# Performance work log

Hardware: AMD Instinct MI355X
Metric: run time of the kernel (lower is better)

The kernel has to match this reference:

```python
import jax, jax.numpy as jnp
import numpy as np
import math

B, S, H, DK = 16, 4096, 16, 64
DM = H * DK          # 1024, d_model
QD = 1024            # q_d_model
KVD = 1024           # kv_d_model
MASK_P = 0.85        # randbool probability


def setup_inputs() -> dict:
    key = jax.random.key(0)
    ks = jax.random.split(key, 12)
    s = 0.02
    return {
        "q": jax.random.normal(ks[0], (B, 1, QD), jnp.float32),
        "k": jax.random.normal(ks[1], (B, S, KVD), jnp.float32),
        "v": jax.random.normal(ks[2], (B, S, KVD), jnp.float32),
        "Wq": jax.random.normal(ks[3], (QD, DM), jnp.float32) * s,
        "bq": jnp.zeros((DM,), jnp.float32),
        "Wk": jax.random.normal(ks[4], (KVD, DM), jnp.float32) * s,
        "bk": jnp.zeros((DM,), jnp.float32),
        "Wv": jax.random.normal(ks[5], (KVD, DM), jnp.float32) * s,
        "bv": jnp.zeros((DM,), jnp.float32),
        "Wo": jax.random.normal(ks[6], (DM, QD), jnp.float32) * s,
        "bo": jnp.zeros((QD,), jnp.float32),
        # randbool(shape, p=0.85): True where rand < p -> score zeroed
        "maskfill": jax.random.uniform(ks[7], (B, H, 1, S)) < MASK_P,
    }


def reference(q, k, v, Wq, bq, Wk, bk, Wv, bv, Wo, bo, maskfill):
    bs = q.shape[0]
    # projections -> [B, L, H, DK] -> [B, H, L, DK]
    qh = (q @ Wq + bq).reshape(bs, -1, H, DK).transpose(0, 2, 1, 3)  # [B,H,1,DK]
    kh = (k @ Wk + bk).reshape(bs, -1, H, DK).transpose(0, 2, 1, 3)  # [B,H,S,DK]
    vh = (v @ Wv + bv).reshape(bs, -1, H, DK).transpose(0, 2, 1, 3)  # [B,H,S,DK]

    scores1 = jnp.einsum("bhqd,bhkd->bhqk", qh, kh) / math.sqrt(DK)  # [B,H,1,S]

    # plain path (dropout = identity in eval)
    attn = jax.nn.softmax(scores1, axis=-1)
    out_h = jnp.einsum("bhqk,bhkd->bhqd", attn, vh)                  # [B,H,1,DK]

    # masked path: zero-fill (not -inf) masked raw scores, then softmax
    masked_scores = jnp.where(maskfill, 0.0, scores1)
    mattn = jax.nn.softmax(masked_scores, axis=-1)
    mout_h = jnp.einsum("bhqk,bhkd->bhqd", mattn, vh)

    concat = out_h.transpose(0, 2, 1, 3).reshape(bs, DM)
    mconcat = mout_h.transpose(0, 2, 1, 3).reshape(bs, DM)
    output = concat @ Wo + bo
    masked_output = mconcat @ Wo + bo
    return (output, masked_output)
```

## Files before the change

kernel.cpp:

```cpp
#include <hip/hip_runtime.h>
#include <stdint.h>

#define NB 16
#define NS 4096
#define NH 16
#define NC 1024

#define OFF_QHP   0u
#define OFF_QK    262144u
#define OFF_QB    524288u
#define OFF_SP    524608u
#define OFF_CTXP  532800u
#define OFF_CON   8921408u

__global__ __launch_bounds__(128) void k_qh(
    const float* __restrict__ q, const float* __restrict__ Wq, float* __restrict__ qhp)
{
    __shared__ float qs[64*16];
    int dz = blockIdx.x, cs = blockIdx.y;
    int tid = threadIdx.x;
    int d = dz*128 + tid;
#pragma unroll
    for (int j = 0; j < 2; ++j) {
        int idx = j*128 + tid;
        int b = idx >> 4, c4 = (idx & 15) << 2;
        float4 t = *(const float4*)(q + (size_t)b*NC + cs*64 + c4);
        qs[(c4+0)*16 + b] = t.x; qs[(c4+1)*16 + b] = t.y;
        qs[(c4+2)*16 + b] = t.z; qs[(c4+3)*16 + b] = t.w;
    }
    __syncthreads();
    float acc[16];
#pragma unroll
    for (int b = 0; b < 16; ++b) acc[b] = 0.f;
#pragma unroll 4
    for (int c = 0; c < 64; ++c) {
        float w = Wq[(size_t)(cs*64 + c)*NC + d];
        const float4* qr = (const float4*)(qs + c*16);
        float4 q0 = qr[0], q1 = qr[1], q2 = qr[2], q3 = qr[3];
        acc[0]  = fmaf(w, q0.x, acc[0]);  acc[1]  = fmaf(w, q0.y, acc[1]);
        acc[2]  = fmaf(w, q0.z, acc[2]);  acc[3]  = fmaf(w, q0.w, acc[3]);
        acc[4]  = fmaf(w, q1.x, acc[4]);  acc[5]  = fmaf(w, q1.y, acc[5]);
        acc[6]  = fmaf(w, q1.z, acc[6]);  acc[7]  = fmaf(w, q1.w, acc[7]);
        acc[8]  = fmaf(w, q2.x, acc[8]);  acc[9]  = fmaf(w, q2.y, acc[9]);
        acc[10] = fmaf(w, q2.z, acc[10]); acc[11] = fmaf(w, q2.w, acc[11]);
        acc[12] = fmaf(w, q3.x, acc[12]); acc[13] = fmaf(w, q3.y, acc[13]);
        acc[14] = fmaf(w, q3.z, acc[14]); acc[15] = fmaf(w, q3.w, acc[15]);
    }
#pragma unroll
    for (int b = 0; b < 16; ++b) qhp[((size_t)cs*16 + b)*NC + d] = acc[b];
}

__global__ __launch_bounds__(128) void k_qk(
    const float* __restrict__ qhp, const float* __restrict__ bq,
    const float* __restrict__ Wk, const float* __restrict__ bk,
    float* __restrict__ qko, float* __restrict__ qbv)
{
    int h = blockIdx.x;
    int c = blockIdx.y*128 + threadIdx.x;
    __shared__ float qs[16*64];
    for (int j = 0; j < 8; ++j) {
        int idx = j*128 + threadIdx.x;
        int b = idx >> 6, dd = idx & 63;
        float a = bq[h*64 + dd];
#pragma unroll
        for (int cs = 0; cs < 16; ++cs) a += qhp[((size_t)cs*16 + b)*NC + h*64 + dd];
        qs[idx] = a;
    }
    __syncthreads();
    const float* wr = Wk + (size_t)c*NC + h*64;
    float acc[16];
#pragma unroll
    for (int b = 0; b < 16; ++b) acc[b] = 0.f;
#pragma unroll 4
    for (int d = 0; d < 64; ++d) {
        float w = wr[d];
#pragma unroll
        for (int b = 0; b < 16; ++b) acc[b] = fmaf(qs[b*64 + d], w, acc[b]);
    }
#pragma unroll
    for (int b = 0; b < 16; ++b) qko[((size_t)b*NH + h)*NC + c] = acc[b];
    if (blockIdx.y == 0 && threadIdx.x < 16) {
        int b = threadIdx.x; float a = 0.f;
        for (int d = 0; d < 64; ++d) a = fmaf(qs[b*64 + d], bk[h*64 + d], a);
        qbv[b*NH + h] = a;
    }
}

#define QTS 20
#define SCOMP(BUF, W)                                                          \
    _Pragma("unroll")                                                          \
    for (int j = 0; j < 4; ++j) {                                              \
        const float* qp = qt + ((W)*16 + ph*4 + j)*QTS + hg*4;                 \
        float4 qv = *(const float4*)qp;                                        \
        _Pragma("unroll")                                                      \
        for (int i = 0; i < 8; ++i) {                                          \
            float kc = (j == 0) ? BUF[i].x : (j == 1) ? BUF[i].y               \
                     : (j == 2) ? BUF[i].z : BUF[i].w;                         \
            acc[i][0] = fmaf(kc, qv.x, acc[i][0]);                             \
            acc[i][1] = fmaf(kc, qv.y, acc[i][1]);                             \
            acc[i][2] = fmaf(kc, qv.z, acc[i][2]);                             \
            acc[i][3] = fmaf(kc, qv.w, acc[i][3]);                             \
        }                                                                      \
    }
__global__ __launch_bounds__(512, 2) void k_att(
    const float* __restrict__ kk, const float* __restrict__ vv,
    const float* __restrict__ qkm, const float* __restrict__ qbv,
    const void* __restrict__ mask, float* __restrict__ ctxp, float* __restrict__ Sp)
{
    __shared__ float qt[512*QTS];
    __shared__ float attl[256*32];
    __shared__ float red[8][2][16];
    int sb = blockIdx.x, b = blockIdx.y;
    int tid = threadIdx.x;
    int ph = tid & 3, hg = (tid >> 2) & 3, rg = tid >> 4;
    int srow = sb*256 + rg*8;

    int fl;
    {
        const uint4* mw = (const uint4*)mask;
        unsigned f = 0u, g = 0u;
#pragma unroll
        for (int j = 0; j < 8; ++j) {
            uint4 m4 = mw[j];
            f |= (m4.x == 0x3F800000u) | (m4.y == 0x3F800000u)
               | (m4.z == 0x3F800000u) | (m4.w == 0x3F800000u);
            g |= ((m4.x > 1u) & (m4.x != 0x3F800000u))
               | ((m4.y > 1u) & (m4.y != 0x3F800000u))
               | ((m4.z > 1u) & (m4.z != 0x3F800000u))
               | ((m4.w > 1u) & (m4.w != 0x3F800000u));
        }
        fl = f ? 2 : (g ? 1 : 0);
    }

    const float* kr = kk + ((size_t)b*NS + srow)*NC + ph*4;
    float acc[8][4];
#pragma unroll
    for (int i = 0; i < 8; ++i)
#pragma unroll
        for (int j = 0; j < 4; ++j) acc[i][j] = 0.f;

    for (int cz = 0; cz < 2; ++cz) {
        __syncthreads();
#pragma unroll
        for (int j = 0; j < 16; ++j) {
            int idx = j*512 + tid;
            int h = idx >> 9, c = idx & 511;
            qt[c*QTS + h] = qkm[((size_t)b*NH + h)*NC + cz*512 + c];
        }
        __syncthreads();
        const float* kc0 = kr + cz*512;
        float4 kv[8], kn[8];
#pragma unroll
        for (int i = 0; i < 8; ++i) kv[i] = *(const float4*)(kc0 + i*NC);
        for (int w = 0; w < 32; ++w) {
            if (w < 31) {
#pragma unroll
                for (int i = 0; i < 8; ++i)
                    kn[i] = *(const float4*)(kc0 + i*NC + (w+1)*16);
            }
            SCOMP(kv, w);
#pragma unroll
            for (int i = 0; i < 8; ++i) kv[i] = kn[i];
        }
    }
#pragma unroll
    for (int i = 0; i < 8; ++i)
#pragma unroll
        for (int j = 0; j < 4; ++j) {
            acc[i][j] += __shfl_xor(acc[i][j], 1, 64);
            acc[i][j] += __shfl_xor(acc[i][j], 2, 64);
        }
    float d0[4], d1[4];
    if (ph == 0) {
#pragma unroll
        for (int j = 0; j < 4; ++j) { d0[j] = acc[0][j]; d1[j] = acc[1][j]; }
    } else if (ph == 1) {
#pragma unroll
        for (int j = 0; j < 4; ++j) { d0[j] = acc[2][j]; d1[j] = acc[3][j]; }
    } else if (ph == 2) {
#pragma unroll
        for (int j = 0; j < 4; ++j) { d0[j] = acc[4][j]; d1[j] = acc[5][j]; }
    } else {
#pragma unroll
        for (int j = 0; j < 4; ++j) { d0[j] = acc[6][j]; d1[j] = acc[7][j]; }
    }
    int lA = rg*8 + 2*ph, lB = lA + 1;
    int sA = sb*256 + lA, sB = sA + 1;
    unsigned mA = 0, mB = 0;
    if (fl == 1) {
        const uint8_t* mp = (const uint8_t*)mask + (size_t)(b*NH + hg*4)*NS;
#pragma unroll
        for (int j = 0; j < 4; ++j) {
            if (mp[(size_t)j*NS + sA]) mA |= (1u << j);
            if (mp[(size_t)j*NS + sB]) mB |= (1u << j);
        }
    } else if (fl == 2) {
        const float* mp = (const float*)mask + (size_t)(b*NH + hg*4)*NS;
#pragma unroll
        for (int j = 0; j < 4; ++j) {
            if (mp[(size_t)j*NS + sA] != 0.f) mA |= (1u << j);
            if (mp[(size_t)j*NS + sB] != 0.f) mB |= (1u << j);
        }
    } else {
        const int* mp = (const int*)mask + (size_t)(b*NH + hg*4)*NS;
#pragma unroll
        for (int j = 0; j < 4; ++j) {
            if (mp[(size_t)j*NS + sA]) mA |= (1u << j);
            if (mp[(size_t)j*NS + sB]) mB |= (1u << j);
        }
    }
    float p0a[4], p1a[4], p0b[4], p1b[4], r0[4], r1[4];
#pragma unroll
    for (int j = 0; j < 4; ++j) {
        float qb = qbv[b*NH + hg*4 + j];
        float va = (d0[j] + qb) * 0.125f;
        float vb = (d1[j] + qb) * 0.125f;
        p0a[j] = __expf(va);  p1a[j] = (mA >> j & 1u) ? 1.0f : p0a[j];
        p0b[j] = __expf(vb);  p1b[j] = (mB >> j & 1u) ? 1.0f : p0b[j];
        r0[j] = p0a[j] + p0b[j];
        r1[j] = p1a[j] + p1b[j];
    }
    {
        int swA = (lA & 7) << 2, swB = (lB & 7) << 2;
        *(float4*)(attl + lA*32 + ((hg*4) ^ swA))        = make_float4(p0a[0], p0a[1], p0a[2], p0a[3]);
        *(float4*)(attl + lA*32 + ((16 + hg*4) ^ swA))   = make_float4(p1a[0], p1a[1], p1a[2], p1a[3]);
        *(float4*)(attl + lB*32 + ((hg*4) ^ swB))        = make_float4(p0b[0], p0b[1], p0b[2], p0b[3]);
        *(float4*)(attl + lB*32 + ((16 + hg*4) ^ swB))   = make_float4(p1b[0], p1b[1], p1b[2], p1b[3]);
    }
#pragma unroll
    for (int j = 0; j < 4; ++j) {
        r0[j] += __shfl_xor(r0[j], 1, 64);  r1[j] += __shfl_xor(r1[j], 1, 64);
        r0[j] += __shfl_xor(r0[j], 2, 64);  r1[j] += __shfl_xor(r1[j], 2, 64);
        r0[j] += __shfl_xor(r0[j], 16, 64); r1[j] += __shfl_xor(r1[j], 16, 64);
        r0[j] += __shfl_xor(r0[j], 32, 64); r1[j] += __shfl_xor(r1[j], 32, 64);
    }
    int wv = tid >> 6;
    if ((tid & 51) == 0) {
#pragma unroll
        for (int j = 0; j < 4; ++j) {
            red[wv][0][hg*4 + j] = r0[j];
            red[wv][1][hg*4 + j] = r1[j];
        }
    }
    __syncthreads();
    if (tid < 32) {
        int pa = tid >> 4, h = tid & 15;
        float a = 0.f;
#pragma unroll
        for (int w8 = 0; w8 < 8; ++w8) a += red[w8][pa][h];
        Sp[((size_t)b*16 + sb)*32 + tid] = a;
    }

    int cq = tid & 255, half = tid >> 8;
    float cacc[32][4];
#pragma unroll
    for (int u = 0; u < 32; ++u)
#pragma unroll
        for (int j = 0; j < 4; ++j) cacc[u][j] = 0.f;
    const float* vb = vv + ((size_t)b*NS + sb*256 + half*128)*NC + cq*4;
    for (int r = 0; r < 128; ++r) {
        float4 vvv = *(const float4*)(vb + (size_t)r*NC);
        int l = half*128 + r;
        const float* ar = attl + l*32;
        int lw = l & 7;
#pragma unroll
        for (int g = 0; g < 8; ++g) {
            float4 aw = *(const float4*)(ar + ((g ^ lw) << 2));
            cacc[g*4+0][0] = fmaf(aw.x, vvv.x, cacc[g*4+0][0]);
            cacc[g*4+0][1] = fmaf(aw.x, vvv.y, cacc[g*4+0][1]);
            cacc[g*4+0][2] = fmaf(aw.x, vvv.z, cacc[g*4+0][2]);
            cacc[g*4+0][3] = fmaf(aw.x, vvv.w, cacc[g*4+0][3]);
            cacc[g*4+1][0] = fmaf(aw.y, vvv.x, cacc[g*4+1][0]);
            cacc[g*4+1][1] = fmaf(aw.y, vvv.y, cacc[g*4+1][1]);
            cacc[g*4+1][2] = fmaf(aw.y, vvv.z, cacc[g*4+1][2]);
            cacc[g*4+1][3] = fmaf(aw.y, vvv.w, cacc[g*4+1][3]);
            cacc[g*4+2][0] = fmaf(aw.z, vvv.x, cacc[g*4+2][0]);
            cacc[g*4+2][1] = fmaf(aw.z, vvv.y, cacc[g*4+2][1]);
            cacc[g*4+2][2] = fmaf(aw.z, vvv.z, cacc[g*4+2][2]);
            cacc[g*4+2][3] = fmaf(aw.z, vvv.w, cacc[g*4+2][3]);
            cacc[g*4+3][0] = fmaf(aw.w, vvv.x, cacc[g*4+3][0]);
            cacc[g*4+3][1] = fmaf(aw.w, vvv.y, cacc[g*4+3][1]);
            cacc[g*4+3][2] = fmaf(aw.w, vvv.z, cacc[g*4+3][2]);
            cacc[g*4+3][3] = fmaf(aw.w, vvv.w, cacc[g*4+3][3]);
        }
    }
    float* buf = qt;
#pragma unroll
    for (int pr = 0; pr < 4; ++pr) {
        __syncthreads();
        if (half == 1) {
#pragma unroll
            for (int u = 0; u < 8; ++u)
                *(float4*)(buf + (u*256 + cq)*4) =
                    make_float4(cacc[pr*8+u][0], cacc[pr*8+u][1],
                                cacc[pr*8+u][2], cacc[pr*8+u][3]);
        }
        __syncthreads();
        if (half == 0) {
#pragma unroll
            for (int u = 0; u < 8; ++u) {
                float4 t = *(const float4*)(buf + (u*256 + cq)*4);
                int uph = pr*8 + u, p = uph >> 4, h = uph & 15;
                float4 s;
                s.x = cacc[pr*8+u][0] + t.x; s.y = cacc[pr*8+u][1] + t.y;
                s.z = cacc[pr*8+u][2] + t.z; s.w = cacc[pr*8+u][3] + t.w;
                *(float4*)(ctxp + ((((size_t)sb*2 + p)*NB + b)*NH + h)*NC + cq*4) = s;
            }
        }
    }
}

__global__ __launch_bounds__(256) void k_outhN(
    const float* __restrict__ ctxp, const float* __restrict__ Sp,
    const float* __restrict__ Wv, const float* __restrict__ bv,
    float* __restrict__ con)
{
    int b = blockIdx.y, p = blockIdx.z;
    int dx = blockIdx.x;
    int d = dx*256 + threadIdx.x;
    int h0 = dx*4;
    __shared__ float cl[4*NC];
    float Sinv[4];
#pragma unroll
    for (int j = 0; j < 4; ++j) {
        float a = 0.f;
        for (int sb = 0; sb < 16; ++sb)
            a += Sp[((size_t)b*16 + sb)*32 + p*16 + h0 + j];
        Sinv[j] = 1.f / a;
    }
#pragma unroll
    for (int hh = 0; hh < 4; ++hh) {
        for (int cc = threadIdx.x; cc < NC; cc += 256) {
            float a = 0.f;
#pragma unroll
            for (int ss = 0; ss < 16; ++ss)
                a += ctxp[((((size_t)ss*2 + p)*NB + b)*NH + h0 + hh)*NC + cc];
            cl[hh*NC + cc] = a * Sinv[hh];
        }
    }
    __syncthreads();
    const float* c2 = cl + ((threadIdx.x >> 6) << 10);
    float a0=0.f,a1=0.f,a2=0.f,a3=0.f;
    for (int c = 0; c < NC; c += 4) {
        a0 = fmaf(c2[c+0], Wv[(size_t)(c+0)*NC + d], a0);
        a1 = fmaf(c2[c+1], Wv[(size_t)(c+1)*NC + d], a1);
        a2 = fmaf(c2[c+2], Wv[(size_t)(c+2)*NC + d], a2);
        a3 = fmaf(c2[c+3], Wv[(size_t)(c+3)*NC + d], a3);
    }
    con[((size_t)p*NB + b)*NC + d] = (a0+a1)+(a2+a3) + bv[d];
}

__global__ __launch_bounds__(256) void k_out(
    const float* __restrict__ con, const float* __restrict__ Wo,
    const float* __restrict__ bo, float* __restrict__ out)
{
    int b = blockIdx.y, p = blockIdx.z;
    int o = blockIdx.x*256 + threadIdx.x;
    __shared__ float cl[NC];
    for (int i = threadIdx.x; i < NC; i += 256)
        cl[i] = con[((size_t)p*NB + b)*NC + i];
    __syncthreads();
    float a0=0.f,a1=0.f,a2=0.f,a3=0.f;
    for (int m = 0; m < NC; m += 4) {
        a0 = fmaf(cl[m+0], Wo[(size_t)(m+0)*NC + o], a0);
        a1 = fmaf(cl[m+1], Wo[(size_t)(m+1)*NC + o], a1);
        a2 = fmaf(cl[m+2], Wo[(size_t)(m+2)*NC + o], a2);
        a3 = fmaf(cl[m+3], Wo[(size_t)(m+3)*NC + o], a3);
    }
    out[(size_t)p*NB*NC + (size_t)b*NC + o] = (a0+a1)+(a2+a3) + bo[o];
}

extern "C" void kernel_launch(void* const* d_in, const int* in_sizes, int n_in,
                              void* d_out, int out_size, void* d_ws, size_t ws_size,
                              hipStream_t stream)
{
    (void)in_sizes; (void)n_in; (void)out_size; (void)ws_size;
    const float* q  = (const float*)d_in[0];
    const float* k  = (const float*)d_in[1];
    const float* v  = (const float*)d_in[2];
    const float* Wq = (const float*)d_in[3];
    const float* bq = (const float*)d_in[4];
    const float* Wk = (const float*)d_in[5];
    const float* bk = (const float*)d_in[6];
    const float* Wv = (const float*)d_in[7];
    const float* bv = (const float*)d_in[8];
    const float* Wo = (const float*)d_in[9];
    const float* bo = (const float*)d_in[10];
    const void*  mk = d_in[11];

    float* ws   = (float*)d_ws;
    float* qhp  = ws + OFF_QHP;
    float* qkv  = ws + OFF_QK;
    float* qbv  = ws + OFF_QB;
    float* Sp   = ws + OFF_SP;
    float* ctxp = ws + OFF_CTXP;
    float* con  = ws + OFF_CON;
    float* out  = (float*)d_out;

    k_qh<<<dim3(8, 16), 128, 0, stream>>>(q, Wq, qhp);
    k_qk<<<dim3(16, 8), 128, 0, stream>>>(qhp, bq, Wk, bk, qkv, qbv);
    k_att<<<dim3(16, 16), 512, 0, stream>>>(k, v, qkv, qbv, mk, ctxp, Sp);
    k_outhN<<<dim3(4, NB, 2), 256, 0, stream>>>(ctxp, Sp, Wv, bv, con);
    k_out<<<dim3(4, NB, 2), 256, 0, stream>>>(con, Wo, bo, out);
}
```

Baseline: 284.3 us.

## Split attention-V accumulation by column group instead of row half; deepen K prefetch

The score loop now keeps two K tiles in flight, using a three-buffer rotation that prefetches two steps ahead. In the context kernel, each half of the block previously covered half of the 256 rows for all 32 (path, head) columns. Now each half covers all 256 rows for 16 columns, one path each, so the shared-memory reduction and its barriers go away and accumulator registers drop from 128 to 64. The cost is that each thread loads V twice as many times (both halves read the same V rows, though L2 should serve the repeats), in exchange for fewer registers and no cross-half reduction.

```diff
diff --git a/kernel.cpp b/kernel.cpp
--- a/kernel.cpp
+++ b/kernel.cpp
@@ -149,18 +149,26 @@
         }
         __syncthreads();
         const float* kc0 = kr + cz*512;
-        float4 kv[8], kn[8];
-#pragma unroll
-        for (int i = 0; i < 8; ++i) kv[i] = *(const float4*)(kc0 + i*NC);
-        for (int w = 0; w < 32; ++w) {
-            if (w < 31) {
+        float4 A[8], B[8], T[8];
+#pragma unroll
+        for (int i = 0; i < 8; ++i) A[i] = *(const float4*)(kc0 + i*NC);
+#pragma unroll
+        for (int i = 0; i < 8; ++i) B[i] = *(const float4*)(kc0 + i*NC + 16);
+        for (int w = 0; w < 32; w += 2) {
+            if (w + 2 < 32) {
 #pragma unroll
                 for (int i = 0; i < 8; ++i)
-                    kn[i] = *(const float4*)(kc0 + i*NC + (w+1)*16);
+                    T[i] = *(const float4*)(kc0 + i*NC + (w+2)*16);
             }
-            SCOMP(kv, w);
-#pragma unroll
-            for (int i = 0; i < 8; ++i) kv[i] = kn[i];
+            SCOMP(A, w);
+            if (w + 3 < 32) {
+#pragma unroll
+                for (int i = 0; i < 8; ++i)
+                    A[i] = *(const float4*)(kc0 + i*NC + (w+3)*16);
+            }
+            SCOMP(B, (w+1));
+#pragma unroll
+            for (int i = 0; i < 8; ++i) { B[i] = A[i]; A[i] = T[i]; }
         }
     }
 #pragma unroll
@@ -252,61 +260,45 @@
     }
 
     int cq = tid & 255, half = tid >> 8;
-    float cacc[32][4];
-#pragma unroll
-    for (int u = 0; u < 32; ++u)
+    float cacc[16][4];
+#pragma unroll
+    for (int u = 0; u < 16; ++u)
 #pragma unroll
         for (int j = 0; j < 4; ++j) cacc[u][j] = 0.f;
-    const float* vb = vv + ((size_t)b*NS + sb*256 + half*128)*NC + cq*4;
-    for (int r = 0; r < 128; ++r) {
-        float4 vvv = *(const float4*)(vb + (size_t)r*NC);
-        int l = half*128 + r;
-        const float* ar = attl + l*32;
-        int lw = l & 7;
-#pragma unroll
-        for (int g = 0; g < 8; ++g) {
-            float4 aw = *(const float4*)(ar + ((g ^ lw) << 2));
-            cacc[g*4+0][0] = fmaf(aw.x, vvv.x, cacc[g*4+0][0]);
-            cacc[g*4+0][1] = fmaf(aw.x, vvv.y, cacc[g*4+0][1]);
-            cacc[g*4+0][2] = fmaf(aw.x, vvv.z, cacc[g*4+0][2]);
-            cacc[g*4+0][3] = fmaf(aw.x, vvv.w, cacc[g*4+0][3]);
-            cacc[g*4+1][0] = fmaf(aw.y, vvv.x, cacc[g*4+1][0]);
-            cacc[g*4+1][1] = fmaf(aw.y, vvv.y, cacc[g*4+1][1]);
-            cacc[g*4+1][2] = fmaf(aw.y, vvv.z, cacc[g*4+1][2]);
-            cacc[g*4+1][3] = fmaf(aw.y, vvv.w, cacc[g*4+1][3]);
-            cacc[g*4+2][0] = fmaf(aw.z, vvv.x, cacc[g*4+2][0]);
-            cacc[g*4+2][1] = fmaf(aw.z, vvv.y, cacc[g*4+2][1]);
-            cacc[g*4+2][2] = fmaf(aw.z, vvv.z, cacc[g*4+2][2]);
-            cacc[g*4+2][3] = fmaf(aw.z, vvv.w, cacc[g*4+2][3]);
-            cacc[g*4+3][0] = fmaf(aw.w, vvv.x, cacc[g*4+3][0]);
-            cacc[g*4+3][1] = fmaf(aw.w, vvv.y, cacc[g*4+3][1]);
-            cacc[g*4+3][2] = fmaf(aw.w, vvv.z, cacc[g*4+3][2]);
-            cacc[g*4+3][3] = fmaf(aw.w, vvv.w, cacc[g*4+3][3]);
-        }
-    }
-    float* buf = qt;
-#pragma unroll
-    for (int pr = 0; pr < 4; ++pr) {
-        __syncthreads();
-        if (half == 1) {
-#pragma unroll
-            for (int u = 0; u < 8; ++u)
-                *(float4*)(buf + (u*256 + cq)*4) =
-                    make_float4(cacc[pr*8+u][0], cacc[pr*8+u][1],
-                                cacc[pr*8+u][2], cacc[pr*8+u][3]);
-        }
-        __syncthreads();
-        if (half == 0) {
-#pragma unroll
-            for (int u = 0; u < 8; ++u) {
-                float4 t = *(const float4*)(buf + (u*256 + cq)*4);
-                int uph = pr*8 + u, p = uph >> 4, h = uph & 15;
-                float4 s;
-                s.x = cacc[pr*8+u][0] + t.x; s.y = cacc[pr*8+u][1] + t.y;
-                s.z = cacc[pr*8+u][2] + t.z; s.w = cacc[pr*8+u][3] + t.w;
-                *(float4*)(ctxp + ((((size_t)sb*2 + p)*NB + b)*NH + h)*NC + cq*4) = s;
-            }
-        }
+    const float* vb = vv + ((size_t)b*NS + sb*256)*NC + cq*4;
+    float4 vcur = *(const float4*)vb;
+    for (int r = 0; r < 256; ++r) {
+        float4 vnxt;
+        if (r < 255) vnxt = *(const float4*)(vb + (size_t)(r+1)*NC);
+        const float* ar = attl + r*32;
+        int lw = r & 7;
+#pragma unroll
+        for (int g = 0; g < 4; ++g) {
+            int G = half*4 + g;
+            float4 aw = *(const float4*)(ar + ((G ^ lw) << 2));
+            cacc[g*4+0][0] = fmaf(aw.x, vcur.x, cacc[g*4+0][0]);
+            cacc[g*4+0][1] = fmaf(aw.x, vcur.y, cacc[g*4+0][1]);
+            cacc[g*4+0][2] = fmaf(aw.x, vcur.z, cacc[g*4+0][2]);
+            cacc[g*4+0][3] = fmaf(aw.x, vcur.w, cacc[g*4+0][3]);
+            cacc[g*4+1][0] = fmaf(aw.y, vcur.x, cacc[g*4+1][0]);
+            cacc[g*4+1][1] = fmaf(aw.y, vcur.y, cacc[g*4+1][1]);
+            cacc[g*4+1][2] = fmaf(aw.y, vcur.z, cacc[g*4+1][2]);
+            cacc[g*4+1][3] = fmaf(aw.y, vcur.w, cacc[g*4+1][3]);
+            cacc[g*4+2][0] = fmaf(aw.z, vcur.x, cacc[g*4+2][0]);
+            cacc[g*4+2][1] = fmaf(aw.z, vcur.y, cacc[g*4+2][1]);
+            cacc[g*4+2][2] = fmaf(aw.z, vcur.z, cacc[g*4+2][2]);
+            cacc[g*4+2][3] = fmaf(aw.z, vcur.w, cacc[g*4+2][3]);
+            cacc[g*4+3][0] = fmaf(aw.w, vcur.x, cacc[g*4+3][0]);
+            cacc[g*4+3][1] = fmaf(aw.w, vcur.y, cacc[g*4+3][1]);
+            cacc[g*4+3][2] = fmaf(aw.w, vcur.z, cacc[g*4+3][2]);
+            cacc[g*4+3][3] = fmaf(aw.w, vcur.w, cacc[g*4+3][3]);
+        }
+        vcur = vnxt;
+    }
+#pragma unroll
+    for (int gh = 0; gh < 16; ++gh) {
+        *(float4*)(ctxp + ((((size_t)sb*2 + half)*NB + b)*NH + gh)*NC + cq*4)
+            = make_float4(cacc[gh][0], cacc[gh][1], cacc[gh][2], cacc[gh][3]);
     }
 }
 
```

After: 289.0 us. About the same (+1.7%).
